# Kernel optimization log

Hardware: AMD Instinct MI355X
Metric: run time of the kernel (lower is better)

The kernel has to match this reference:

```python
import jax, jax.numpy as jnp
import numpy as np

B, S, SE = 4, 1024, 1024
E, H, M = 768, 12, 100
D = E // H
EPS = 1e-5
GELU_C = 0.7978845608028654  # sqrt(2/pi)


def _ln(x, g, b):
    mu = x.mean(-1, keepdims=True)
    v = ((x - mu) ** 2).mean(-1, keepdims=True)
    return g * (x - mu) / jnp.sqrt(v + EPS) + b


def _gelu(x):
    return 0.5 * x * (1.0 + jnp.tanh(GELU_C * (x + 0.044715 * x ** 3)))


def _split(x):  # [b,s,E] -> [b,H,s,D]
    b, s, _ = x.shape
    return x.reshape(b, s, H, D).transpose(0, 2, 1, 3)


def _merge(x):  # [b,H,s,D] -> [b,s,E]
    b, h, s, d = x.shape
    return x.transpose(0, 2, 1, 3).reshape(b, s, h * d)


def _forward(x, encoder_features, ln1_g, ln1_b, ln2_g, ln2_b,
             c_attn_w, c_attn_b, attn_proj_w, attn_proj_b,
             memory_features, mem_attn_w, mem_attn_b, mem_alpha_w, mem_alpha_b,
             fcq_w, fcq_b, fck_w, fck_b, fcv_w, fcv_b, enc_proj_w, enc_proj_b,
             fc_alpha1_w, fc_alpha1_b, fc_alpha2_w, fc_alpha2_b,
             mlp_fc_w, mlp_fc_b, mlp_proj_w, mlp_proj_b, mask_encoder):
    # ---- memory-augmented self-attention (note: original has NO 1/sqrt(d) scaling here) ----
    h = _ln(x, ln1_g, ln1_b)
    qkv = h @ c_attn_w + c_attn_b
    q, k, v = jnp.split(qkv, 3, axis=-1)
    q, k, v = _split(q), _split(k), _split(v)
    w = jax.nn.softmax(jnp.einsum('bhqd,bhkd->bhqk', q, k), axis=-1)
    a = _merge(jnp.einsum('bhqk,bhkd->bhqd', w, v))
    # memory slots are batch-independent -> compute once, broadcast over batch
    mem = memory_features[0] @ mem_attn_w + mem_attn_b  # [M, 2E]
    mk, mv = jnp.split(mem, 2, axis=-1)
    mk = mk.reshape(M, H, D).transpose(1, 2, 0)  # [H,D,M]
    mv = mv.reshape(M, H, D).transpose(1, 0, 2)  # [H,M,D]
    wm = jax.nn.softmax(jnp.einsum('bhqd,hdm->bhqm', q, mk), axis=-1)
    a1 = _merge(jnp.einsum('bhqm,hmd->bhqd', wm, mv))
    al = jax.nn.sigmoid(jnp.concatenate([a, a1], -1) @ mem_alpha_w + mem_alpha_b)
    a = al * a + (1.0 - al) * a1
    a = a @ attn_proj_w + attn_proj_b
    a = x + a  # residual (dropout = identity in eval)

    # ---- two cross-attentions sharing weights and ln_1 ----
    ha = _ln(a, ln1_g, ln1_b)

    def enc_dec(enc):
        qe = _split(ha @ fcq_w + fcq_b)
        ke = _split(enc @ fck_w + fck_b)
        ve = _split(enc @ fcv_w + fcv_b)
        we = jnp.einsum('bhqd,bhkd->bhqk', qe, ke) / np.float32(np.sqrt(D))
        we = jnp.where(mask_encoder, jnp.float32(-10000.0), we)
        we = jax.nn.softmax(we, axis=-1)
        o = _merge(jnp.einsum('bhqk,bhkd->bhqd', we, ve))
        return o @ enc_proj_w + enc_proj_b

    e1 = enc_dec(_ln(encoder_features[:, 0], ln1_g, ln1_b))
    e2 = enc_dec(_ln(encoder_features[:, 1], ln1_g, ln1_b))
    al1 = jax.nn.sigmoid(jnp.concatenate([a, e1], -1) @ fc_alpha1_w + fc_alpha1_b)
    al2 = jax.nn.sigmoid(jnp.concatenate([a, e2], -1) @ fc_alpha2_w + fc_alpha2_b)
    e1 = al1 * a + (1.0 - al1) * e1
    e2 = al2 * a + (1.0 - al2) * e2
    a = (e1 + e2) / np.float32(np.sqrt(2.0))

    # ---- MLP ----
    hm = _ln(a, ln2_g, ln2_b)
    m = _gelu(hm @ mlp_fc_w + mlp_fc_b) @ mlp_proj_w + mlp_proj_b
    return a + m


def setup_inputs() -> dict:
    key = jax.random.key(0)
    ks = iter(jax.random.split(key, 48))

    def rn(shape, s=0.02):
        return jax.random.normal(next(ks), shape, jnp.float32) * s

    return dict(
        x=jax.random.normal(next(ks), (B, S, E), jnp.float32),
        encoder_features=jax.random.normal(next(ks), (B, 2, SE, E), jnp.float32),
        mask_encoder=jax.random.bernoulli(next(ks), 0.1, (B, 1, 1, SE)),
        ln1_g=jnp.ones(E, jnp.float32), ln1_b=jnp.zeros(E, jnp.float32),
        ln2_g=jnp.ones(E, jnp.float32), ln2_b=jnp.zeros(E, jnp.float32),
        c_attn_w=rn((E, 3 * E)), c_attn_b=jnp.zeros(3 * E, jnp.float32),
        attn_proj_w=rn((E, E)), attn_proj_b=jnp.zeros(E, jnp.float32),
        memory_features=rn((1, M, E), 1.0),
        mem_attn_w=rn((E, 2 * E)), mem_attn_b=jnp.zeros(2 * E, jnp.float32),
        mem_alpha_w=rn((2 * E, E)), mem_alpha_b=jnp.zeros(E, jnp.float32),
        fcq_w=rn((E, E)), fcq_b=jnp.zeros(E, jnp.float32),
        fck_w=rn((E, E)), fck_b=jnp.zeros(E, jnp.float32),
        fcv_w=rn((E, E)), fcv_b=jnp.zeros(E, jnp.float32),
        enc_proj_w=rn((E, E)), enc_proj_b=jnp.zeros(E, jnp.float32),
        fc_alpha1_w=rn((2 * E, E)), fc_alpha1_b=jnp.zeros(E, jnp.float32),
        fc_alpha2_w=rn((2 * E, E)), fc_alpha2_b=jnp.zeros(E, jnp.float32),
        mlp_fc_w=rn((E, 4 * E)), mlp_fc_b=jnp.zeros(4 * E, jnp.float32),
        mlp_proj_w=rn((4 * E, E)), mlp_proj_b=jnp.zeros(E, jnp.float32),
    )


def reference(x, encoder_features, mask_encoder, ln1_g, ln1_b, ln2_g, ln2_b,
              c_attn_w, c_attn_b, attn_proj_w, attn_proj_b,
              memory_features, mem_attn_w, mem_attn_b, mem_alpha_w, mem_alpha_b,
              fcq_w, fcq_b, fck_w, fck_b, fcv_w, fcv_b, enc_proj_w, enc_proj_b,
              fc_alpha1_w, fc_alpha1_b, fc_alpha2_w, fc_alpha2_b,
              mlp_fc_w, mlp_fc_b, mlp_proj_w, mlp_proj_b):
    return _forward(x, encoder_features, ln1_g, ln1_b, ln2_g, ln2_b,
                    c_attn_w, c_attn_b, attn_proj_w, attn_proj_b,
                    memory_features, mem_attn_w, mem_attn_b, mem_alpha_w, mem_alpha_b,
                    fcq_w, fcq_b, fck_w, fck_b, fcv_w, fcv_b, enc_proj_w, enc_proj_b,
                    fc_alpha1_w, fc_alpha1_b, fc_alpha2_w, fc_alpha2_b,
                    mlp_fc_w, mlp_fc_b, mlp_proj_w, mlp_proj_b, mask_encoder)
```

## Files before the change

### kernel.cpp

```cpp
#include <hip/hip_runtime.h>

typedef __bf16 bf16_t;
typedef __bf16 bf16x8v __attribute__((ext_vector_type(8)));
typedef float f32x4 __attribute__((ext_vector_type(4)));

#define CB 4
#define CE 768
#define CH 12
#define CD 64

__device__ __forceinline__ void gload16(const void* g, void* l) {
    __builtin_amdgcn_global_load_lds((const __attribute__((address_space(1))) void*)g,
                                     (__attribute__((address_space(3))) void*)l, 16, 0, 0);
}

__device__ __forceinline__ void xcd_remap(int& bx, int& by, int gx, int gy) {
    int nwg = gx * gy;
    if ((nwg & 7) == 0) {
        int lin = by * gx + bx;
        int lin2 = (lin & 7) * (nwg >> 3) + (lin >> 3);
        bx = lin2 % gx;
        by = lin2 / gx;
    }
}

template<int BM, int BN, int CONCAT, int ACT, int RES, int OUT, int CMODE>
__global__ __launch_bounds__(256)
void gemm_n(const bf16_t* __restrict__ A0, const bf16_t* __restrict__ A1,
            const bf16_t* __restrict__ Bt, const float* __restrict__ bias,
            const float* __restrict__ bias2, const void* __restrict__ resid,
            void* __restrict__ C, void* __restrict__ C2, void* __restrict__ C3,
            int M, int N, int K, int lda, int ldc)
{
    constexpr int WM = BM / 2, WN = BN / 2, RM = WM / 16, RN = WN / 16;
    __shared__ __align__(16) bf16_t As0[BM * 64], As1[BM * 64];
    __shared__ __align__(16) bf16_t Bs0[BN * 64], Bs1[BN * 64];

    const int t = threadIdx.x;
    const int lane = t & 63, wave = t >> 6;
    int bx = blockIdx.x, by = blockIdx.y;
    xcd_remap(bx, by, gridDim.x, gridDim.y);
    const int m0 = by * BM, n0 = bx * BN;
    const int wm = (wave & 1) * WM, wn = (wave >> 1) * WN;
    const int fr = lane & 15, quad = lane >> 4;

    const int lr = lane >> 3;
    const int kof = ((lane & 7) ^ lr) * 8;

    const bf16_t* A1b = A1;
    if (CMODE == 6) A1b = A1 + (n0 >= 768 ? (long)4096 * 768 : 0);

    f32x4 acc[RM][RN];
#pragma unroll
    for (int i = 0; i < RM; i++)
#pragma unroll
        for (int j = 0; j < RN; j++)
#pragma unroll
            for (int p = 0; p < 4; p++) acc[i][j][p] = 0.f;

    auto stage = [&](bf16_t* As, bf16_t* Bs, int kt) {
        const bf16_t* Ab = A0;
        int kk = kt;
        if (CONCAT && kt >= 768) { Ab = A1b; kk = kt - 768; }
        const bf16_t* asrc = Ab + (long)(m0 + wave * 8 + lr) * lda + kk + kof;
#pragma unroll
        for (int c = 0; c < BM / 32; ++c)
            gload16(asrc + (long)c * 32 * lda, &As[(c * 32 + wave * 8) * 64]);
        const bf16_t* bsrc = Bt + (long)(n0 + wave * 8 + lr) * K + kt + kof;
#pragma unroll
        for (int c = 0; c < BN / 32; ++c)
            gload16(bsrc + (long)c * 32 * K, &Bs[(c * 32 + wave * 8) * 64]);
    };

    const int sw = fr & 7;
    auto compute = [&](const bf16_t* As, const bf16_t* Bs) {
        bf16x8v af[RM][2], bfr[RN][2];
        const int s0 = quad ^ sw;
#pragma unroll
        for (int i = 0; i < RM; ++i) {
            const char* rb = (const char*)As + (wm + i * 16 + fr) * 128;
            af[i][0] = *(const bf16x8v*)(rb + (s0 << 4));
            af[i][1] = *(const bf16x8v*)(rb + ((s0 ^ 4) << 4));
        }
#pragma unroll
        for (int j = 0; j < RN; ++j) {
            const char* rb = (const char*)Bs + (wn + j * 16 + fr) * 128;
            bfr[j][0] = *(const bf16x8v*)(rb + (s0 << 4));
            bfr[j][1] = *(const bf16x8v*)(rb + ((s0 ^ 4) << 4));
        }
#pragma unroll
        for (int ks = 0; ks < 2; ++ks)
#pragma unroll
            for (int i = 0; i < RM; ++i)
#pragma unroll
                for (int j = 0; j < RN; ++j)
                    acc[i][j] = __builtin_amdgcn_mfma_f32_16x16x32_bf16(af[i][ks], bfr[j][ks], acc[i][j], 0, 0, 0);
    };

    const int nk = K >> 6;
    stage(As0, Bs0, 0);
    __syncthreads();
    for (int kt = 0; kt + 2 <= nk; kt += 2) {
        stage(As1, Bs1, (kt + 1) << 6);
        compute(As0, Bs0);
        __syncthreads();
        if (kt + 2 < nk) stage(As0, Bs0, (kt + 2) << 6);
        compute(As1, Bs1);
        __syncthreads();
    }

    const int rq = quad * 4, cn = fr;
#pragma unroll
    for (int i = 0; i < RM; i++)
#pragma unroll
        for (int j = 0; j < RN; j++) {
            int col = n0 + wn + j * 16 + cn;
            int t3 = (CMODE == 4 || CMODE == 5) ? (col / 768) : 0;
            int cc = col - t3 * 768;
            float bv = 0.f;
            if (CMODE == 5)      bv = t3 ? bias2[cc] : bias[cc];
            else if (CMODE == 6) bv = (col < 768) ? bias[col] : bias2[col - 768];
            else if (bias)       bv = bias[col];
            const int row0 = m0 + wm + i * 16 + rq;
            float vv[4];
#pragma unroll
            for (int p = 0; p < 4; p++) {
                float v = acc[i][j][p] + bv;
                if (ACT == 1) v = 1.f / (1.f + __expf(-v));
                if (ACT == 2) {
                    float u2 = 1.5957691216057308f * (v + 0.044715f * v * v * v);
                    v = v / (1.f + __expf(-u2));
                }
                if (RES == 2) v += ((const float*)resid)[(long)(row0 + p) * ldc + col];
                vv[p] = v;
            }
            if (CMODE == 0) {
#pragma unroll
                for (int p = 0; p < 4; p++) {
                    long idx = (long)(row0 + p) * ldc + col;
                    if (OUT == 0)      ((bf16_t*)C)[idx] = (bf16_t)vv[p];
                    else if (OUT == 1) ((float*)C)[idx] = vv[p];
                    else { ((float*)C)[idx] = vv[p]; ((bf16_t*)C2)[idx] = (bf16_t)vv[p]; }
                }
            } else if (CMODE == 6) {
                long base = (col < 768) ? 0 : ((long)4096 * 768 - 768);
#pragma unroll
                for (int p = 0; p < 4; p++)
                    ((bf16_t*)C)[base + (long)(row0 + p) * 768 + col] = (bf16_t)vv[p];
            } else {
                int bb = row0 >> 10, ss0 = row0 & 1023;
                int hh = cc >> 6, dd = cc & 63;
                long srow = (long)(bb * CH + hh) * 1024 + ss0;
                long tbase = (((long)(bb * CH + hh) * 64) + dd) * 1024 + ss0;
                union { ushort4 u4; bf16_t b[4]; } pk;
#pragma unroll
                for (int p = 0; p < 4; p++) pk.b[p] = (bf16_t)vv[p];
                if (CMODE == 2) {
#pragma unroll
                    for (int p = 0; p < 4; p++)
                        ((bf16_t*)C)[(srow + p) * 64 + dd] = pk.b[p];
                } else if (CMODE == 5) {
                    if (t3 == 0) {
#pragma unroll
                        for (int p = 0; p < 4; p++)
                            ((bf16_t*)C)[(srow + p) * 64 + dd] = pk.b[p];
                    } else {
                        *(ushort4*)((bf16_t*)C2 + tbase) = pk.u4;
                    }
                } else {
                    if (t3 == 0) {
#pragma unroll
                        for (int p = 0; p < 4; p++)
                            ((bf16_t*)C)[(srow + p) * 64 + dd] = pk.b[p];
                    } else if (t3 == 1) {
#pragma unroll
                        for (int p = 0; p < 4; p++)
                            ((bf16_t*)C2)[(srow + p) * 64 + dd] = pk.b[p];
                    } else {
                        *(ushort4*)((bf16_t*)C3 + tbase) = pk.u4;
                    }
                }
            }
        }
}

template<int MODE>
__global__ __launch_bounds__(256)
void flash_attn(const bf16_t* __restrict__ Q, const bf16_t* __restrict__ K,
                const bf16_t* __restrict__ V, const int* __restrict__ mask,
                bf16_t* __restrict__ O)
{
    __shared__ __align__(16) bf16_t Qs[64 * 72];
    __shared__ __align__(16) bf16_t Ks0[64 * 64], Ks1[64 * 64];
    __shared__ __align__(16) bf16_t Vs0[64 * 64], Vs1[64 * 64];

    const int t = threadIdx.x;
    const int lane = t & 63, wave = t >> 6;
    int bx = blockIdx.x, bz = blockIdx.z;
    {
        int nwg = gridDim.x * gridDim.z;
        if ((nwg & 7) == 0) {
            int lin = bz * gridDim.x + bx;
            int lin2 = (lin & 7) * (nwg >> 3) + (lin >> 3);
            bx = lin2 % gridDim.x;
            bz = lin2 / gridDim.x;
        }
    }
    const int b = bz / CH, h = bz % CH;
    const int q0 = bx * 64;

    const bf16_t* Qb = Q + (long)bz * (1024 * 64) + (long)q0 * 64;
    const bf16_t* Kb = (MODE == 2) ? K + (long)h * (128 * 64) : K + (long)bz * (1024 * 64);
    const bf16_t* Vb = (MODE == 2) ? V + (long)h * (64 * 128) : V + (long)bz * (64 * 1024);
    const int ldv = (MODE == 2) ? 128 : 1024;
    const int NT = (MODE == 2) ? 2 : 16;

    const int lr = lane >> 3, kof = ((lane & 7) ^ lr) * 8;

    auto stageKV = [&](bf16_t* Ks, bf16_t* Vs, int kt) {
#pragma unroll
        for (int c = 0; c < 2; ++c) {
            int r = wave * 8 + c * 32;
            gload16(Kb + (long)(kt * 64 + r + lr) * 64 + kof, &Ks[r * 64]);
            gload16(Vb + (long)(r + lr) * ldv + kt * 64 + kof, &Vs[r * 64]);
        }
    };

    stageKV(Ks0, Vs0, 0);
    const int r0 = t >> 3, c0 = (t & 7) * 8;
    for (int rr = r0; rr < 64; rr += 32)
        *(uint4*)&Qs[rr * 72 + c0] = *(const uint4*)&Qb[(long)rr * 64 + c0];
    __syncthreads();

    const int fr = lane & 15, quad = lane >> 4;
    const int sw = fr & 7;
    bf16x8v qf[2];
#pragma unroll
    for (int ks = 0; ks < 2; ks++)
        qf[ks] = *(const bf16x8v*)&Qs[(wave * 16 + fr) * 72 + quad * 8 + ks * 32];

    bf16_t* Ps = &Qs[wave * 16 * 72];

    f32x4 o[4];
    float mrow[4], lrow[4];
#pragma unroll
    for (int p = 0; p < 4; p++) { mrow[p] = -1e30f; lrow[p] = 0.f; }
#pragma unroll
    for (int j = 0; j < 4; j++)
#pragma unroll
        for (int p = 0; p < 4; p++) o[j][p] = 0.f;

    auto tile = [&](const bf16_t* Ks, const bf16_t* Vs, int kt) {
        f32x4 s[4];
#pragma unroll
        for (int j = 0; j < 4; j++)
#pragma unroll
            for (int p = 0; p < 4; p++) s[j][p] = 0.f;
#pragma unroll
        for (int ks = 0; ks < 2; ks++) {
            bf16x8v bk[4];
#pragma unroll
            for (int j = 0; j < 4; j++) {
                const char* rb = (const char*)Ks + (j * 16 + fr) * 128;
                bk[j] = *(const bf16x8v*)(rb + (((quad ^ sw) ^ (ks << 2)) << 4));
            }
#pragma unroll
            for (int j = 0; j < 4; j++)
                s[j] = __builtin_amdgcn_mfma_f32_16x16x32_bf16(qf[ks], bk[j], s[j], 0, 0, 0);
        }
        if (MODE == 1) {
#pragma unroll
            for (int j = 0; j < 4; j++) {
                int mv = mask[(long)b * 1024 + kt * 64 + j * 16 + fr];
#pragma unroll
                for (int p = 0; p < 4; p++)
                    s[j][p] = mv ? -10000.f : s[j][p] * 0.125f;
            }
        }
        if (MODE == 2) {
#pragma unroll
            for (int j = 0; j < 4; j++)
                if (kt * 64 + j * 16 + fr >= 100)
#pragma unroll
                    for (int p = 0; p < 4; p++) s[j][p] = -1e30f;
        }
#pragma unroll
        for (int p = 0; p < 4; p++) {
            float tm = fmaxf(fmaxf(s[0][p], s[1][p]), fmaxf(s[2][p], s[3][p]));
            tm = fmaxf(tm, __shfl_xor(tm, 1, 64));
            tm = fmaxf(tm, __shfl_xor(tm, 2, 64));
            tm = fmaxf(tm, __shfl_xor(tm, 4, 64));
            tm = fmaxf(tm, __shfl_xor(tm, 8, 64));
            float mnew = fmaxf(mrow[p], tm);
            float alpha = __expf(mrow[p] - mnew);
            mrow[p] = mnew;
            float rs = 0.f;
#pragma unroll
            for (int j = 0; j < 4; j++) {
                float e = __expf(s[j][p] - mnew);
                s[j][p] = e;
                rs += e;
            }
            rs += __shfl_xor(rs, 1, 64);
            rs += __shfl_xor(rs, 2, 64);
            rs += __shfl_xor(rs, 4, 64);
            rs += __shfl_xor(rs, 8, 64);
            lrow[p] = lrow[p] * alpha + rs;
#pragma unroll
            for (int j = 0; j < 4; j++) o[j][p] *= alpha;
        }
#pragma unroll
        for (int j = 0; j < 4; j++)
#pragma unroll
            for (int p = 0; p < 4; p++)
                Ps[(quad * 4 + p) * 72 + j * 16 + fr] = (bf16_t)s[j][p];
#pragma unroll
        for (int ks = 0; ks < 2; ks++) {
            bf16x8v af = *(const bf16x8v*)&Ps[fr * 72 + quad * 8 + ks * 32];
            bf16x8v bv[4];
#pragma unroll
            for (int j = 0; j < 4; j++) {
                const char* rb = (const char*)Vs + (j * 16 + fr) * 128;
                bv[j] = *(const bf16x8v*)(rb + (((quad ^ sw) ^ (ks << 2)) << 4));
            }
#pragma unroll
            for (int j = 0; j < 4; j++)
                o[j] = __builtin_amdgcn_mfma_f32_16x16x32_bf16(af, bv[j], o[j], 0, 0, 0);
        }
    };

    for (int kt = 0; kt + 2 <= NT; kt += 2) {
        stageKV(Ks1, Vs1, kt + 1);
        tile(Ks0, Vs0, kt);
        __syncthreads();
        if (kt + 2 < NT) stageKV(Ks0, Vs0, kt + 2);
        tile(Ks1, Vs1, kt + 1);
        __syncthreads();
    }
#pragma unroll
    for (int p = 0; p < 4; p++) {
        float inv = 1.f / lrow[p];
        int srow = q0 + wave * 16 + quad * 4 + p;
        long base = ((long)b * 1024 + srow) * 768 + h * 64;
#pragma unroll
        for (int j = 0; j < 4; j++)
            O[base + j * 16 + fr] = (bf16_t)(o[j][p] * inv);
    }
}

__device__ __forceinline__ void ln_body(const float* in, bf16_t* out,
                                        const float* g, const float* b,
                                        long base, long ob, int t)
{
    __shared__ float red[4];
    float v0 = in[base + t], v1 = in[base + t + 256], v2 = in[base + t + 512];
    float s = v0 + v1 + v2;
    for (int m = 32; m; m >>= 1) s += __shfl_xor(s, m, 64);
    if ((t & 63) == 0) red[t >> 6] = s;
    __syncthreads();
    s = red[0] + red[1] + red[2] + red[3];
    __syncthreads();
    const float mu = s * (1.f / 768.f);
    float d0 = v0 - mu, d1 = v1 - mu, d2 = v2 - mu;
    float q = d0 * d0 + d1 * d1 + d2 * d2;
    for (int m = 32; m; m >>= 1) q += __shfl_xor(q, m, 64);
    if ((t & 63) == 0) red[t >> 6] = q;
    __syncthreads();
    q = red[0] + red[1] + red[2] + red[3];
    const float rstd = rsqrtf(q * (1.f / 768.f) + 1e-5f);
    out[ob + t]       = (bf16_t)(g[t]       * d0 * rstd + b[t]);
    out[ob + t + 256] = (bf16_t)(g[t + 256] * d1 * rstd + b[t + 256]);
    out[ob + t + 512] = (bf16_t)(g[t + 512] * d2 * rstd + b[t + 512]);
}

__global__ __launch_bounds__(256)
void ln_kernel(const float* __restrict__ in, bf16_t* __restrict__ out,
               const float* __restrict__ g, const float* __restrict__ b)
{
    const int r = blockIdx.x;
    ln_body(in, out, g, b, (long)r * CE, (long)r * CE, threadIdx.x);
}

__global__ __launch_bounds__(256)
void ln_enc(const float* __restrict__ encf, bf16_t* __restrict__ out,
            const float* __restrict__ g, const float* __restrict__ b)
{
    const int r = blockIdx.x;
    const int e = r >> 12, rr = r & 4095, bb = rr >> 10, s = rr & 1023;
    ln_body(encf, out, g, b, ((long)(bb * 2 + e) * 1024 + s) * CE, (long)r * CE, threadIdx.x);
}

__global__ void blend_kernel(const bf16_t* __restrict__ al, bf16_t* __restrict__ a,
                             const bf16_t* __restrict__ a1)
{
    int idx = blockIdx.x * 256 + threadIdx.x;
    float g = (float)al[idx];
    a[idx] = (bf16_t)(g * (float)a[idx] + (1.f - g) * (float)a1[idx]);
}

__global__ void fuse_gates2(const bf16_t* __restrict__ gal, const bf16_t* __restrict__ eo,
                            float* __restrict__ rf)
{
    const long SZel = (long)4096 * 768;
    long idx = (long)blockIdx.x * 256 + threadIdx.x;
    float g1 = (float)gal[idx], g2 = (float)gal[idx + SZel];
    float e1 = (float)eo[idx],  e2 = (float)eo[idx + SZel];
    float r = rf[idx];
    float v = g1 * r + (1.f - g1) * e1 + g2 * r + (1.f - g2) * e2;
    rf[idx] = v * 0.7071067811865476f;
}

__global__ void zero_out(float* __restrict__ out)
{
    out[blockIdx.x * 256 + threadIdx.x] = 0.f;
}

__global__ void transpose_cast(const float* __restrict__ in, bf16_t* __restrict__ out,
                               int K, int N)
{
    __shared__ bf16_t tile[32][33];
    int n0 = blockIdx.x * 32, k0 = blockIdx.y * 32;
    int tx = threadIdx.x, ty = threadIdx.y;
    for (int i = ty; i < 32; i += 8)
        tile[i][tx] = (bf16_t)in[(long)(k0 + i) * N + n0 + tx];
    __syncthreads();
    for (int i = ty; i < 32; i += 8)
        out[(long)(n0 + i) * K + k0 + tx] = tile[tx][i];
}

__global__ void cast_pad_mem(const float* __restrict__ memf, bf16_t* __restrict__ out)
{
    int idx = blockIdx.x * 256 + threadIdx.x;
    int row = idx / 768;
    out[idx] = (row < 100) ? (bf16_t)memf[idx] : (bf16_t)0.f;
}

__global__ void repack_mem(const bf16_t* __restrict__ mem, bf16_t* __restrict__ mkt,
                           bf16_t* __restrict__ mvt)
{
    int idx = blockIdx.x * 256 + threadIdx.x;
    int d = idx & 63;
    int slot = (idx >> 6) & 127;
    int h = idx >> 13;
    bf16_t kv = (slot < 100) ? mem[slot * 1536 + h * CD + d] : (bf16_t)0.f;
    bf16_t vv = (slot < 100) ? mem[slot * 1536 + CE + h * CD + d] : (bf16_t)0.f;
    mkt[idx] = kv;
    mvt[((long)h * 64 + d) * 128 + slot] = vv;
}

extern "C" void kernel_launch(void* const* d_in, const int* in_sizes, int n_in,
                              void* d_out, int out_size, void* d_ws, size_t ws_size,
                              hipStream_t stream)
{
    (void)in_sizes; (void)n_in; (void)out_size;
    const float* x        = (const float*)d_in[0];
    const float* encf     = (const float*)d_in[1];
    const int*   maskenc  = (const int*)d_in[2];
    const float* ln1_g    = (const float*)d_in[3];
    const float* ln1_b    = (const float*)d_in[4];
    const float* ln2_g    = (const float*)d_in[5];
    const float* ln2_b    = (const float*)d_in[6];
    const float* c_attn_w = (const float*)d_in[7];
    const float* c_attn_b = (const float*)d_in[8];
    const float* aproj_w  = (const float*)d_in[9];
    const float* aproj_b  = (const float*)d_in[10];
    const float* memf     = (const float*)d_in[11];
    const float* mattn_w  = (const float*)d_in[12];
    const float* mattn_b  = (const float*)d_in[13];
    const float* malpha_w = (const float*)d_in[14];
    const float* malpha_b = (const float*)d_in[15];
    const float* fcq_w    = (const float*)d_in[16];
    const float* fcq_b    = (const float*)d_in[17];
    const float* fck_w    = (const float*)d_in[18];
    const float* fck_b    = (const float*)d_in[19];
    const float* fcv_w    = (const float*)d_in[20];
    const float* fcv_b    = (const float*)d_in[21];
    const float* eproj_w  = (const float*)d_in[22];
    const float* eproj_b  = (const float*)d_in[23];
    const float* fa1_w    = (const float*)d_in[24];
    const float* fa1_b    = (const float*)d_in[25];
    const float* fa2_w    = (const float*)d_in[26];
    const float* fa2_b    = (const float*)d_in[27];
    const float* mfc_w    = (const float*)d_in[28];
    const float* mfc_b    = (const float*)d_in[29];
    const float* mproj_w  = (const float*)d_in[30];
    const float* mproj_b  = (const float*)d_in[31];
    float* dout = (float*)d_out;

    size_t off = 0;
    auto alloc = [&](size_t bytes) -> void* {
        void* p = (char*)d_ws + off;
        off = (off + bytes + 255) & ~(size_t)255;
        return p;
    };
    const size_t SZ = (size_t)4096 * 768 * 2;
    const long SZel = (long)4096 * 768;
    bf16_t* wt_cattn  = (bf16_t*)alloc((size_t)2304 * 768 * 2);
    bf16_t* wt_aproj  = (bf16_t*)alloc((size_t)768 * 768 * 2);
    bf16_t* wt_malpha = (bf16_t*)alloc((size_t)768 * 1536 * 2);
    bf16_t* wt_fcq    = (bf16_t*)alloc((size_t)768 * 768 * 2);
    bf16_t* wt_fck    = (bf16_t*)alloc((size_t)768 * 768 * 2);
    bf16_t* wt_fcv    = (bf16_t*)alloc((size_t)768 * 768 * 2);
    bf16_t* wt_eproj  = (bf16_t*)alloc((size_t)768 * 768 * 2);
    bf16_t* wt_fa1    = (bf16_t*)alloc((size_t)768 * 1536 * 2);
    bf16_t* wt_fa2    = (bf16_t*)alloc((size_t)768 * 1536 * 2);
    bf16_t* wt_mfc    = (bf16_t*)alloc((size_t)3072 * 768 * 2);
    bf16_t* wt_mproj  = (bf16_t*)alloc((size_t)768 * 3072 * 2);
    bf16_t* wt_mattn  = (bf16_t*)alloc((size_t)1536 * 768 * 2);
    bf16_t* memb   = (bf16_t*)alloc((size_t)128 * 768 * 2);
    bf16_t* membuf = (bf16_t*)alloc((size_t)128 * 1536 * 2);
    bf16_t* mkt    = (bf16_t*)alloc((size_t)CH * 128 * 64 * 2);
    bf16_t* mvt    = (bf16_t*)alloc((size_t)CH * 64 * 128 * 2);
    bf16_t* bufA   = (bf16_t*)alloc(SZ);
    bf16_t* qbuf   = (bf16_t*)alloc(SZ);
    bf16_t* kbuf   = (bf16_t*)alloc(2 * SZ);
    bf16_t* vtbuf  = (bf16_t*)alloc(2 * SZ);
    bf16_t* asbuf  = (bf16_t*)alloc(2 * SZ);
    bf16_t* bufB   = (bf16_t*)alloc(2 * SZ);
    float*  residf = (float*)alloc((size_t)4096 * 768 * 4);
    bf16_t* residb = (bf16_t*)alloc(SZ);

    if (off > ws_size) {
        zero_out<<<12288, 256, 0, stream>>>(dout);
        return;
    }
    bf16_t* mid = kbuf;
    bf16_t* galbuf = kbuf;
    bf16_t* eobuf = bufB;

    const dim3 blk(256);

    auto T = [&](const float* w, bf16_t* wt, int Kd, int Nd) {
        transpose_cast<<<dim3(Nd / 32, Kd / 32), dim3(32, 8), 0, stream>>>(w, wt, Kd, Nd);
    };
    T(c_attn_w, wt_cattn, 768, 2304);
    T(aproj_w, wt_aproj, 768, 768);
    T(malpha_w, wt_malpha, 1536, 768);
    T(fcq_w, wt_fcq, 768, 768);
    T(fck_w, wt_fck, 768, 768);
    T(fcv_w, wt_fcv, 768, 768);
    T(eproj_w, wt_eproj, 768, 768);
    T(fa1_w, wt_fa1, 1536, 768);
    T(fa2_w, wt_fa2, 1536, 768);
    T(mfc_w, wt_mfc, 768, 3072);
    T(mproj_w, wt_mproj, 3072, 768);
    T(mattn_w, wt_mattn, 768, 1536);

    cast_pad_mem<<<384, blk, 0, stream>>>(memf, memb);
    gemm_n<64,64,0,0,0,0,0><<<dim3(24, 2), blk, 0, stream>>>(
        memb, nullptr, wt_mattn, mattn_b, nullptr, nullptr, membuf, nullptr, nullptr,
        128, 1536, 768, 768, 1536);
    repack_mem<<<384, blk, 0, stream>>>(membuf, mkt, mvt);

    ln_kernel<<<4096, blk, 0, stream>>>(x, bufA, ln1_g, ln1_b);
    gemm_n<128,128,0,0,0,0,4><<<dim3(18, 32), blk, 0, stream>>>(
        bufA, nullptr, wt_cattn, c_attn_b, nullptr, nullptr, qbuf, kbuf, vtbuf,
        4096, 2304, 768, 768, 0);

    flash_attn<0><<<dim3(16, 1, 48), blk, 0, stream>>>(qbuf, kbuf, vtbuf, nullptr, asbuf);
    flash_attn<2><<<dim3(16, 1, 48), blk, 0, stream>>>(qbuf, mkt, mvt, nullptr, asbuf + SZel);

    gemm_n<128,64,1,1,0,0,0><<<dim3(12, 32), blk, 0, stream>>>(
        asbuf, asbuf + SZel, wt_malpha, malpha_b, nullptr, nullptr, bufA, nullptr, nullptr,
        4096, 768, 1536, 768, 768);
    blend_kernel<<<12288, blk, 0, stream>>>(bufA, asbuf, asbuf + SZel);
    gemm_n<128,64,0,0,2,2,0><<<dim3(12, 32), blk, 0, stream>>>(
        asbuf, nullptr, wt_aproj, aproj_b, nullptr, x, residf, residb, nullptr,
        4096, 768, 768, 768, 768);

    ln_kernel<<<4096, blk, 0, stream>>>(residf, bufA, ln1_g, ln1_b);
    gemm_n<128,64,0,0,0,0,2><<<dim3(12, 32), blk, 0, stream>>>(
        bufA, nullptr, wt_fcq, fcq_b, nullptr, nullptr, qbuf, nullptr, nullptr,
        4096, 768, 768, 768, 0);

    ln_enc<<<8192, blk, 0, stream>>>(encf, bufB, ln1_g, ln1_b);
    gemm_n<128,128,0,0,0,0,5><<<dim3(12, 64), blk, 0, stream>>>(
        bufB, nullptr, wt_fck, fck_b, fcv_b, nullptr, kbuf, vtbuf, nullptr,
        8192, 1536, 768, 768, 0);
    flash_attn<1><<<dim3(16, 1, 48), blk, 0, stream>>>(
        qbuf, kbuf, vtbuf, maskenc, asbuf);
    flash_attn<1><<<dim3(16, 1, 48), blk, 0, stream>>>(
        qbuf, kbuf + SZel, vtbuf + SZel, maskenc, asbuf + SZel);
    gemm_n<128,128,0,0,0,0,0><<<dim3(6, 64), blk, 0, stream>>>(
        asbuf, nullptr, wt_eproj, eproj_b, nullptr, nullptr, eobuf, nullptr, nullptr,
        8192, 768, 768, 768, 768);
    gemm_n<128,64,1,1,0,0,6><<<dim3(24, 32), blk, 0, stream>>>(
        residb, eobuf, wt_fa1, fa1_b, fa2_b, nullptr, galbuf, nullptr, nullptr,
        4096, 1536, 1536, 768, 768);
    fuse_gates2<<<12288, blk, 0, stream>>>(galbuf, eobuf, residf);

    ln_kernel<<<4096, blk, 0, stream>>>(residf, bufA, ln2_g, ln2_b);
    gemm_n<128,128,0,2,0,0,0><<<dim3(24, 32), blk, 0, stream>>>(
        bufA, nullptr, wt_mfc, mfc_b, nullptr, nullptr, mid, nullptr, nullptr,
        4096, 3072, 768, 768, 3072);
    gemm_n<128,64,0,0,2,1,0><<<dim3(12, 32), blk, 0, stream>>>(
        mid, nullptr, wt_mproj, mproj_b, nullptr, residf, dout, nullptr, nullptr,
        4096, 768, 3072, 3072, 768);
}
```

Baseline: 655.4 us.

## Restructure flash attention: exp2 softmax, lazy rescale, split K/V staging, merged launches

Flash attention now folds log2(e) into the score scale so it can use exp2. The running max is only rescaled when a tile's max exceeds the old max by more than a threshold (lazy rescaling). K and V staging are split: V gets a single buffer loaded while QK^T runs, with extra barriers between the softmax and PV phases. This lowers LDS use but adds synchronisation per tile. The two cross-attention launches are merged into one grid of 96 z-blocks, with an output offset per encoder, to cut launch overhead and improve occupancy.

```diff
diff --git a/kernel.cpp b/kernel.cpp
--- a/kernel.cpp
+++ b/kernel.cpp
@@ -8,6 +8,8 @@
 #define CE 768
 #define CH 12
 #define CD 64
+
+__device__ __forceinline__ float fexp2(float x) { return __builtin_amdgcn_exp2f(x); }
 
 __device__ __forceinline__ void gload16(const void* g, void* l) {
     __builtin_amdgcn_global_load_lds((const __attribute__((address_space(1))) void*)g,
@@ -192,7 +194,7 @@
 {
     __shared__ __align__(16) bf16_t Qs[64 * 72];
     __shared__ __align__(16) bf16_t Ks0[64 * 64], Ks1[64 * 64];
-    __shared__ __align__(16) bf16_t Vs0[64 * 64], Vs1[64 * 64];
+    __shared__ __align__(16) bf16_t Vs[64 * 64];
 
     const int t = threadIdx.x;
     const int lane = t & 63, wave = t >> 6;
@@ -206,27 +208,36 @@
             bz = lin2 / gridDim.x;
         }
     }
-    const int b = bz / CH, h = bz % CH;
+    const int zq = (MODE == 1) ? (bz % 48) : bz;
+    const int b = zq / CH, h = bz % CH;
+    const long eoff = (MODE == 1) ? (long)(bz / 48) * ((long)4096 * 768) : 0;
     const int q0 = bx * 64;
 
-    const bf16_t* Qb = Q + (long)bz * (1024 * 64) + (long)q0 * 64;
-    const bf16_t* Kb = (MODE == 2) ? K + (long)h * (128 * 64) : K + (long)bz * (1024 * 64);
-    const bf16_t* Vb = (MODE == 2) ? V + (long)h * (64 * 128) : V + (long)bz * (64 * 1024);
+    const bf16_t* Qb = Q + (long)zq * 65536 + (long)q0 * 64;
+    const bf16_t* Kb = (MODE == 2) ? K + (long)h * (128 * 64) : K + (long)bz * 65536;
+    const bf16_t* Vb = (MODE == 2) ? V + (long)h * (64 * 128) : V + (long)bz * 65536;
     const int ldv = (MODE == 2) ? 128 : 1024;
     const int NT = (MODE == 2) ? 2 : 16;
+    constexpr float SCL = (MODE == 1) ? 0.18033688011112042f : 1.4426950408889634f;
 
     const int lr = lane >> 3, kof = ((lane & 7) ^ lr) * 8;
 
-    auto stageKV = [&](bf16_t* Ks, bf16_t* Vs, int kt) {
+    auto stageK = [&](bf16_t* Ks, int kt) {
 #pragma unroll
         for (int c = 0; c < 2; ++c) {
             int r = wave * 8 + c * 32;
             gload16(Kb + (long)(kt * 64 + r + lr) * 64 + kof, &Ks[r * 64]);
+        }
+    };
+    auto stageV = [&](int kt) {
+#pragma unroll
+        for (int c = 0; c < 2; ++c) {
+            int r = wave * 8 + c * 32;
             gload16(Vb + (long)(r + lr) * ldv + kt * 64 + kof, &Vs[r * 64]);
         }
     };
 
-    stageKV(Ks0, Vs0, 0);
+    stageK(Ks0, 0);
     const int r0 = t >> 3, c0 = (t & 7) * 8;
     for (int rr = r0; rr < 64; rr += 32)
         *(uint4*)&Qs[rr * 72 + c0] = *(const uint4*)&Qb[(long)rr * 64 + c0];
@@ -250,7 +261,7 @@
 #pragma unroll
         for (int p = 0; p < 4; p++) o[j][p] = 0.f;
 
-    auto tile = [&](const bf16_t* Ks, const bf16_t* Vs, int kt) {
+    auto qkt_sm = [&](const bf16_t* Ks, int kt) {
         f32x4 s[4];
 #pragma unroll
         for (int j = 0; j < 4; j++)
@@ -274,16 +285,19 @@
                 int mv = mask[(long)b * 1024 + kt * 64 + j * 16 + fr];
 #pragma unroll
                 for (int p = 0; p < 4; p++)
-                    s[j][p] = mv ? -10000.f : s[j][p] * 0.125f;
+                    s[j][p] = mv ? -14426.95f : s[j][p] * SCL;
             }
-        }
-        if (MODE == 2) {
+        } else {
 #pragma unroll
             for (int j = 0; j < 4; j++)
-                if (kt * 64 + j * 16 + fr >= 100)
-#pragma unroll
-                    for (int p = 0; p < 4; p++) s[j][p] = -1e30f;
-        }
+#pragma unroll
+                for (int p = 0; p < 4; p++) {
+                    s[j][p] *= SCL;
+                    if (MODE == 2 && kt * 64 + j * 16 + fr >= 100) s[j][p] = -1e30f;
+                }
+        }
+        float tmax[4];
+        bool need = false;
 #pragma unroll
         for (int p = 0; p < 4; p++) {
             float tm = fmaxf(fmaxf(s[0][p], s[1][p]), fmaxf(s[2][p], s[3][p]));
@@ -291,13 +305,26 @@
             tm = fmaxf(tm, __shfl_xor(tm, 2, 64));
             tm = fmaxf(tm, __shfl_xor(tm, 4, 64));
             tm = fmaxf(tm, __shfl_xor(tm, 8, 64));
-            float mnew = fmaxf(mrow[p], tm);
-            float alpha = __expf(mrow[p] - mnew);
-            mrow[p] = mnew;
+            tmax[p] = tm;
+            need = need || (tm > mrow[p] + 8.f);
+        }
+        if (__any(need ? 1 : 0)) {
+#pragma unroll
+            for (int p = 0; p < 4; p++) {
+                float mnew = fmaxf(mrow[p], tmax[p]);
+                float alpha = fexp2(mrow[p] - mnew);
+                lrow[p] *= alpha;
+#pragma unroll
+                for (int j = 0; j < 4; j++) o[j][p] *= alpha;
+                mrow[p] = mnew;
+            }
+        }
+#pragma unroll
+        for (int p = 0; p < 4; p++) {
             float rs = 0.f;
 #pragma unroll
             for (int j = 0; j < 4; j++) {
-                float e = __expf(s[j][p] - mnew);
+                float e = fexp2(s[j][p] - mrow[p]);
                 s[j][p] = e;
                 rs += e;
             }
@@ -305,15 +332,16 @@
             rs += __shfl_xor(rs, 2, 64);
             rs += __shfl_xor(rs, 4, 64);
             rs += __shfl_xor(rs, 8, 64);
-            lrow[p] = lrow[p] * alpha + rs;
-#pragma unroll
-            for (int j = 0; j < 4; j++) o[j][p] *= alpha;
+            lrow[p] += rs;
         }
 #pragma unroll
         for (int j = 0; j < 4; j++)
 #pragma unroll
             for (int p = 0; p < 4; p++)
                 Ps[(quad * 4 + p) * 72 + j * 16 + fr] = (bf16_t)s[j][p];
+    };
+
+    auto pv = [&]() {
 #pragma unroll
         for (int ks = 0; ks < 2; ks++) {
             bf16x8v af = *(const bf16x8v*)&Ps[fr * 72 + quad * 8 + ks * 32];
@@ -329,19 +357,25 @@
         }
     };
 
-    for (int kt = 0; kt + 2 <= NT; kt += 2) {
-        stageKV(Ks1, Vs1, kt + 1);
-        tile(Ks0, Vs0, kt);
+    for (int kt = 0; kt < NT; kt += 2) {
+        stageV(kt);
+        if (kt + 1 < NT) stageK(Ks1, kt + 1);
+        qkt_sm(Ks0, kt);
         __syncthreads();
-        if (kt + 2 < NT) stageKV(Ks0, Vs0, kt + 2);
-        tile(Ks1, Vs1, kt + 1);
+        pv();
+        __syncthreads();
+        stageV(kt + 1);
+        if (kt + 2 < NT) stageK(Ks0, kt + 2);
+        qkt_sm(Ks1, kt + 1);
+        __syncthreads();
+        pv();
         __syncthreads();
     }
 #pragma unroll
     for (int p = 0; p < 4; p++) {
         float inv = 1.f / lrow[p];
         int srow = q0 + wave * 16 + quad * 4 + p;
-        long base = ((long)b * 1024 + srow) * 768 + h * 64;
+        long base = ((long)b * 1024 + srow) * 768 + h * 64 + eoff;
 #pragma unroll
         for (int j = 0; j < 4; j++)
             O[base + j * 16 + fr] = (bf16_t)(o[j][p] * inv);
@@ -577,10 +611,8 @@
     gemm_n<128,128,0,0,0,0,5><<<dim3(12, 64), blk, 0, stream>>>(
         bufB, nullptr, wt_fck, fck_b, fcv_b, nullptr, kbuf, vtbuf, nullptr,
         8192, 1536, 768, 768, 0);
-    flash_attn<1><<<dim3(16, 1, 48), blk, 0, stream>>>(
+    flash_attn<1><<<dim3(16, 1, 96), blk, 0, stream>>>(
         qbuf, kbuf, vtbuf, maskenc, asbuf);
-    flash_attn<1><<<dim3(16, 1, 48), blk, 0, stream>>>(
-        qbuf, kbuf + SZel, vtbuf + SZel, maskenc, asbuf + SZel);
     gemm_n<128,128,0,0,0,0,0><<<dim3(6, 64), blk, 0, stream>>>(
         asbuf, nullptr, wt_eproj, eproj_b, nullptr, nullptr, eobuf, nullptr, nullptr,
         8192, 768, 768, 768, 768);
```

After: 651.0 us. No clear change (-0.7%).
